# Kernel optimization log

Measured on AMD Instinct MI355X. Metric: run time of the kernel, lower is better.

The kernel has to match this reference:

```python
import jax, jax.numpy as jnp
import numpy as np
import math

N = 50000      # nodes
E = 800000     # edges (avg degree 16)
T = 4          # time steps
F = 64         # feature dim (in = hidden = out)
MAX_LEN = 200  # positional encoding table length
EPS = 1e-5     # BatchNorm eps


def _make_pe(time_dim, max_len):
    pe = np.zeros((max_len, time_dim), dtype=np.float32)
    position = np.arange(max_len, dtype=np.float32)[:, None]
    div_term = np.exp(np.arange(0, time_dim, 2, dtype=np.float32) * (-math.log(10000.0) / time_dim))
    pe[:, 0::2] = np.sin(position * div_term)
    pe[:, 1::2] = np.cos(position * div_term)
    return jnp.asarray(pe)


def setup_inputs() -> dict:
    key = jax.random.key(0)
    ks = jax.random.split(key, 10)
    xav = math.sqrt(2.0 / (F + F))  # xavier_normal_ std for square linear
    return {
        "node_features": jax.random.normal(ks[0], (N, T, F), dtype=jnp.float32),
        "edges_weight": jax.random.uniform(ks[1], (T, E), dtype=jnp.float32),
        "identities": jax.random.randint(ks[2], (T,), 0, MAX_LEN),
        "edge_src": jax.random.randint(ks[3], (E,), 0, N),
        "edge_dst": jax.random.randint(ks[4], (E,), 0, N),
        "pe": _make_pe(F, MAX_LEN),
        "W0": jax.random.normal(ks[5], (F, F), dtype=jnp.float32) * xav,
        "W1": jax.random.normal(ks[6], (F, F), dtype=jnp.float32) * xav,
        "g0": jnp.ones((F,), jnp.float32),
        "b0": jnp.zeros((F,), jnp.float32),
        "g1": jnp.ones((F,), jnp.float32),
        "b1": jnp.zeros((F,), jnp.float32),
    }


def _gcn_layer(h, ew, edge_src, edge_dst, W):
    # gather-mul-scatter: msg_e = h[src_e] * w_e ; agg_v = sum_{e: dst=v} msg_e
    msg = h[edge_src] * ew                                   # (E, T, F)
    agg = jax.ops.segment_sum(msg, edge_dst, num_segments=N)  # (N, T, F)
    readout = agg.mean(axis=0)                                # dgl.mean_nodes (single graph) -> (T, F)
    return agg @ W, readout @ W


def _batchnorm(x, gamma, beta):
    # training-mode batch stats over all non-channel dims
    mean = x.mean(axis=(0, 1))
    var = x.var(axis=(0, 1))
    return (x - mean) * jax.lax.rsqrt(var + EPS) * gamma + beta


def reference(node_features, edges_weight, identities, edge_src, edge_dst,
              pe, W0, W1, g0, b0, g1, b1):
    # positional encoding added per time step
    h = node_features + pe[identities]          # (N, T, F)
    ew = edges_weight.T[:, :, None]             # (E, T, 1)
    # layer 0: gcn -> dropout(eval=identity) -> BN -> ReLU
    h, readout = _gcn_layer(h, ew, edge_src, edge_dst, W0)
    h = jax.nn.relu(_batchnorm(h, g0, b0))
    # layer 1 (output layer)
    h, readout = _gcn_layer(h, ew, edge_src, edge_dst, W1)
    h = jax.nn.relu(_batchnorm(h, g1, b1))
    return h, readout
```

## Files before the change

### kernel.cpp

```cpp
#include <hip/hip_runtime.h>

#define TF 256

typedef __attribute__((ext_vector_type(8))) short short8;
typedef __attribute__((ext_vector_type(4))) float f32x4;

__device__ inline unsigned short f2bf(float x) {
  unsigned u = __float_as_uint(x);
  u += 0x7fffu + ((u >> 16) & 1u);
  return (unsigned short)(u >> 16);
}
__device__ inline unsigned pack2(unsigned short lo, unsigned short hi) {
  return (unsigned)lo | ((unsigned)hi << 16);
}
__device__ inline float bflo(unsigned u) { return __uint_as_float(u << 16); }
__device__ inline float bfhi(unsigned u) { return __uint_as_float(u & 0xffff0000u); }

__global__ void zero_kernel(int* __restrict__ p, int n) {
  int i = blockIdx.x * blockDim.x + threadIdx.x;
  if (i < n) p[i] = 0;
}

__global__ void hist_kernel(const int* __restrict__ dst, int* __restrict__ indeg, int E) {
  int e = blockIdx.x * blockDim.x + threadIdx.x;
  if (e < E) atomicAdd(&indeg[dst[e]], 1);
}

__global__ __launch_bounds__(1024) void scan_part1(const int* __restrict__ indeg,
                                                   int* __restrict__ partials, int n) {
  __shared__ int wsum[16];
  const int tid = threadIdx.x;
  const int lane = tid & 63;
  const int wid = tid >> 6;
  int i = blockIdx.x * 1024 + tid;
  int s = (i < n) ? indeg[i] : 0;
  #pragma unroll
  for (int o = 1; o < 64; o <<= 1) s += __shfl_xor(s, o, 64);
  if (lane == 0) wsum[wid] = s;
  __syncthreads();
  if (tid == 0) {
    int acc = 0;
    #pragma unroll
    for (int w = 0; w < 16; ++w) acc += wsum[w];
    partials[blockIdx.x] = acc;
  }
}

__global__ __launch_bounds__(64) void scan_part2(const int* __restrict__ partials,
                                                 int* __restrict__ base,
                                                 int* __restrict__ offsets, int nb, int n) {
  const int i = threadIdx.x;
  int v = (i < nb) ? partials[i] : 0;
  int s = v;
  #pragma unroll
  for (int o = 1; o < 64; o <<= 1) {
    int t = __shfl_up(s, o, 64);
    if (i >= o) s += t;
  }
  if (i < nb) base[i] = s - v;
  if (i == nb - 1) offsets[n] = s;
}

__global__ __launch_bounds__(1024) void scan_part3(const int* __restrict__ indeg,
                                                   const int* __restrict__ base,
                                                   int* __restrict__ offsets,
                                                   int* __restrict__ cursor, int n) {
  __shared__ int wsum[16];
  const int tid = threadIdx.x;
  const int lane = tid & 63;
  const int wid = tid >> 6;
  int i = blockIdx.x * 1024 + tid;
  int v = (i < n) ? indeg[i] : 0;
  int s = v;
  #pragma unroll
  for (int o = 1; o < 64; o <<= 1) {
    int t = __shfl_up(s, o, 64);
    if (lane >= o) s += t;
  }
  if (lane == 63) wsum[wid] = s;
  __syncthreads();
  if (tid == 0) {
    int acc = 0;
    #pragma unroll
    for (int w = 0; w < 16; ++w) { int t = wsum[w]; wsum[w] = acc; acc += t; }
  }
  __syncthreads();
  int excl = s - v + wsum[wid] + base[blockIdx.x];
  if (i < n) { offsets[i] = excl; cursor[i] = excl; }
}

__global__ void fill_kernel(const int* __restrict__ src, const int* __restrict__ dst,
                            const float* __restrict__ ew, int* __restrict__ cursor,
                            int* __restrict__ csr_srcB, float4* __restrict__ csr_w, int E) {
  int e = blockIdx.x * blockDim.x + threadIdx.x;
  if (e >= E) return;
  int d = dst[e];
  int pos = atomicAdd(&cursor[d], 1);
  csr_srcB[pos] = src[e] << 9;
  float4 w;
  w.x = ew[0 * E + e];
  w.y = ew[1 * E + e];
  w.z = ew[2 * E + e];
  w.w = ew[3 * E + e];
  csr_w[pos] = w;
}

__global__ void prep_kernel(const float* __restrict__ x, const float* __restrict__ pe,
                            const int* __restrict__ ids, uint2* __restrict__ h0, int n4) {
  int i = blockIdx.x * blockDim.x + threadIdx.x;
  const int stride = gridDim.x * blockDim.x;
  for (; i < n4; i += stride) {
    int e0 = (i << 2) & (TF - 1);
    int t = e0 >> 6;
    int f4 = e0 & 63;
    float4 v = reinterpret_cast<const float4*>(x)[i];
    float4 p = *reinterpret_cast<const float4*>(&pe[ids[t] * 64 + f4]);
    uint2 o;
    o.x = pack2(f2bf(v.x + p.x), f2bf(v.y + p.y));
    o.y = pack2(f2bf(v.z + p.z), f2bf(v.w + p.w));
    h0[i] = o;
  }
}

template <int LAYER>
__global__ __launch_bounds__(256) void aggregate_kernel(
    const char* __restrict__ h_base, const int* __restrict__ offsets,
    const int* __restrict__ csr_srcB, const float* __restrict__ csr_w,
    const float* __restrict__ scale, const float* __restrict__ shiftv,
    uint4* __restrict__ agg, int n_nodes) {
  const int lane = threadIdx.x & 63;
  const int wid = threadIdx.x >> 6;
  const int v = blockIdx.x * 4 + wid;
  if (v >= n_nodes) return;
  const int p = lane >> 5;
  const unsigned q = lane & 31;
  const unsigned qb = q << 4;
  const int tw = q >> 3;

  float sc[8], sh[8];
  if (LAYER == 1) {
    const int f0 = (q & 7) << 3;
    #pragma unroll
    for (int j = 0; j < 8; ++j) { sc[j] = scale[f0 + j]; sh[j] = shiftv[f0 + j]; }
  }

  float acc[8];
  #pragma unroll
  for (int j = 0; j < 8; ++j) acc[j] = 0.f;

  auto body = [&](uint4 u, float w) {
    float x[8] = {bflo(u.x), bfhi(u.x), bflo(u.y), bfhi(u.y),
                  bflo(u.z), bfhi(u.z), bflo(u.w), bfhi(u.w)};
    #pragma unroll
    for (int j = 0; j < 8; ++j) {
      float t = x[j];
      if (LAYER == 1) t = fmaxf(0.f, fmaf(t, sc[j], sh[j]));
      acc[j] = fmaf(w, t, acc[j]);
    }
  };

  const int beg = offsets[v];
  const int end = offsets[v + 1];
  int i = beg;
  for (; i + 4 <= end; i += 4) {
    const int e0 = i + p;
    const int e1 = i + 2 + p;
    const unsigned s0 = (unsigned)csr_srcB[e0];
    const unsigned s1 = (unsigned)csr_srcB[e1];
    const float w0 = csr_w[e0 * 4 + tw];
    const float w1 = csr_w[e1 * 4 + tw];
    const uint4 u0 = *reinterpret_cast<const uint4*>(h_base + (s0 + qb));
    const uint4 u1 = *reinterpret_cast<const uint4*>(h_base + (s1 + qb));
    body(u0, w0);
    body(u1, w1);
  }
  for (; i < end; i += 2) {
    const int ee = i + p;
    const int e = ee < end ? ee : end - 1;
    float w = csr_w[e * 4 + tw];
    if (ee >= end) w = 0.f;
    const unsigned s = (unsigned)csr_srcB[e];
    const uint4 u = *reinterpret_cast<const uint4*>(h_base + (s + qb));
    body(u, w);
  }

  #pragma unroll
  for (int j = 0; j < 8; ++j) acc[j] += __shfl_xor(acc[j], 32, 64);
  if (lane < 32) {
    uint4 o;
    o.x = pack2(f2bf(acc[0]), f2bf(acc[1]));
    o.y = pack2(f2bf(acc[2]), f2bf(acc[3]));
    o.z = pack2(f2bf(acc[4]), f2bf(acc[5]));
    o.w = pack2(f2bf(acc[6]), f2bf(acc[7]));
    agg[(size_t)v * 32 + q] = o;
  }
}

__global__ __launch_bounds__(512) void wfrag_kernel(const float* __restrict__ W0,
                                                    const float* __restrict__ W1,
                                                    short* __restrict__ wf0,
                                                    short* __restrict__ wf1) {
  const int frag = threadIdx.x >> 6, lane = threadIdx.x & 63;
  const int c = frag >> 1, h = frag & 1;
  const int n = (c << 4) + (lane & 15);
  const int k0 = h * 32 + ((lane >> 4) << 3);
  short* o0 = wf0 + frag * 512 + lane * 8;
  short* o1 = wf1 + frag * 512 + lane * 8;
  #pragma unroll
  for (int i = 0; i < 8; ++i) {
    o0[i] = (short)f2bf(W0[(k0 + i) * 64 + n]);
    o1[i] = (short)f2bf(W1[(k0 + i) * 64 + n]);
  }
}

__global__ __launch_bounds__(256) void mfma_matmul_kernel(
    const unsigned short* __restrict__ aggb, const short* __restrict__ wf,
    unsigned short* __restrict__ y_bf, float* __restrict__ part, int R) {
  const int tid = threadIdx.x;
  const int lane = tid & 63;
  const int wid = tid >> 6;

  short8 bfr[8];
  #pragma unroll
  for (int g = 0; g < 8; ++g)
    bfr[g] = *reinterpret_cast<const short8*>(wf + g * 512 + lane * 8);

  f32x4 csum[4];
  float ssq[4];
  #pragma unroll
  for (int c = 0; c < 4; ++c) { csum[c] = (f32x4){0.f, 0.f, 0.f, 0.f}; ssq[c] = 0.f; }

  const int nrb = (R + 15) >> 4;
  const int k0 = (lane >> 4) << 3;
  for (int rb = blockIdx.x * 4 + wid; rb < nrb; rb += gridDim.x * 4) {
    const int base = rb << 4;
    const int row = base + (lane & 15);
    short8 a0 = (short8){0, 0, 0, 0, 0, 0, 0, 0};
    short8 a1 = a0;
    if (row < R) {
      const short8* ap = reinterpret_cast<const short8*>(aggb + (size_t)row * 64 + k0);
      a0 = ap[0];
      a1 = ap[4];
    }
    f32x4 acc[4];
    #pragma unroll
    for (int c = 0; c < 4; ++c) {
      acc[c] = (f32x4){0.f, 0.f, 0.f, 0.f};
      acc[c] = __builtin_amdgcn_mfma_f32_16x16x32_bf16(a0, bfr[c * 2 + 0], acc[c], 0, 0, 0);
      acc[c] = __builtin_amdgcn_mfma_f32_16x16x32_bf16(a1, bfr[c * 2 + 1], acc[c], 0, 0, 0);
    }
    const int rbase = base + ((lane >> 4) << 2);
    #pragma unroll
    for (int c = 0; c < 4; ++c) {
      const int col = (c << 4) + (lane & 15);
      #pragma unroll
      for (int i = 0; i < 4; ++i) {
        const int r2 = rbase + i;
        if (r2 < R) {
          const float val = acc[c][i];
          y_bf[(size_t)r2 * 64 + col] = f2bf(val);
          csum[c][i] += val;
          ssq[c] += val * val;
        }
      }
    }
  }

  #pragma unroll
  for (int c = 0; c < 4; ++c) {
    #pragma unroll
    for (int i = 0; i < 4; ++i) {
      float v = csum[c][i];
      v += __shfl_xor(v, 16, 64);
      v += __shfl_xor(v, 32, 64);
      csum[c][i] = v;
    }
    float q = ssq[c];
    q += __shfl_xor(q, 16, 64);
    q += __shfl_xor(q, 32, 64);
    ssq[c] = q;
  }
  __shared__ float lcs[4][256];
  __shared__ float lsq[4][64];
  if (lane < 16) {
    #pragma unroll
    for (int c = 0; c < 4; ++c) {
      #pragma unroll
      for (int i = 0; i < 4; ++i) lcs[wid][i * 64 + (c << 4) + lane] = csum[c][i];
      lsq[wid][(c << 4) + lane] = ssq[c];
    }
  }
  __syncthreads();
  float s = lcs[0][tid] + lcs[1][tid] + lcs[2][tid] + lcs[3][tid];
  part[(size_t)blockIdx.x * 320 + tid] = s;
  if (tid < 64)
    part[(size_t)blockIdx.x * 320 + 256 + tid] =
        lsq[0][tid] + lsq[1][tid] + lsq[2][tid] + lsq[3][tid];
}

__global__ __launch_bounds__(1024) void reduce_part_kernel(const float* __restrict__ part,
                                                           float* __restrict__ red, int nblk) {
  __shared__ float lds[1024];
  const int tid = threadIdx.x;
  const int col = blockIdx.x * 16 + (tid & 15);
  const int r = tid >> 4;
  float s = 0.f;
  for (int bk = r; bk < nblk; bk += 64) s += part[(size_t)bk * 320 + col];
  lds[tid] = s;
  __syncthreads();
  #pragma unroll
  for (int off = 512; off >= 16; off >>= 1) {
    if (tid < off) lds[tid] += lds[tid + off];
    __syncthreads();
  }
  if (tid < 16) red[col] = lds[tid];
}

__global__ __launch_bounds__(64) void bn_from_red_kernel(
    const float* __restrict__ red, const float* __restrict__ g, const float* __restrict__ b,
    float* __restrict__ scale, float* __restrict__ shiftv, float inv_count) {
  const int f = threadIdx.x;
  float sum = red[f] + red[64 + f] + red[128 + f] + red[192 + f];
  float mean = sum * inv_count;
  float var = red[256 + f] * inv_count - mean * mean;
  float sc = g[f] * rsqrtf(var + 1e-5f);
  scale[f] = sc;
  shiftv[f] = fmaf(-mean, sc, b[f]);
}

__global__ __launch_bounds__(256) void finalize_from_red_kernel(
    const float* __restrict__ red, const float* __restrict__ g, const float* __restrict__ b,
    float* __restrict__ scale, float* __restrict__ shiftv, float inv_count,
    float* __restrict__ out_readout, float invN) {
  const int tid = threadIdx.x;
  out_readout[tid] = red[tid] * invN;
  if (tid < 64) {
    float sum = red[tid] + red[64 + tid] + red[128 + tid] + red[192 + tid];
    float mean = sum * inv_count;
    float var = red[256 + tid] * inv_count - mean * mean;
    float sc = g[tid] * rsqrtf(var + 1e-5f);
    scale[tid] = sc;
    shiftv[tid] = fmaf(-mean, sc, b[tid]);
  }
}

__global__ void bn_relu_out_kernel(const uint4* __restrict__ yb,
                                   const float* __restrict__ scale,
                                   const float* __restrict__ shiftv,
                                   float4* __restrict__ out, int n8) {
  int i = blockIdx.x * blockDim.x + threadIdx.x;
  if (i >= n8) return;
  const int f0 = (i & 7) << 3;
  uint4 u = yb[i];
  float x[8] = {bflo(u.x), bfhi(u.x), bflo(u.y), bfhi(u.y),
                bflo(u.z), bfhi(u.z), bflo(u.w), bfhi(u.w)};
  float4 o0, o1;
  o0.x = fmaxf(0.f, fmaf(x[0], scale[f0 + 0], shiftv[f0 + 0]));
  o0.y = fmaxf(0.f, fmaf(x[1], scale[f0 + 1], shiftv[f0 + 1]));
  o0.z = fmaxf(0.f, fmaf(x[2], scale[f0 + 2], shiftv[f0 + 2]));
  o0.w = fmaxf(0.f, fmaf(x[3], scale[f0 + 3], shiftv[f0 + 3]));
  o1.x = fmaxf(0.f, fmaf(x[4], scale[f0 + 4], shiftv[f0 + 4]));
  o1.y = fmaxf(0.f, fmaf(x[5], scale[f0 + 5], shiftv[f0 + 5]));
  o1.z = fmaxf(0.f, fmaf(x[6], scale[f0 + 6], shiftv[f0 + 6]));
  o1.w = fmaxf(0.f, fmaf(x[7], scale[f0 + 7], shiftv[f0 + 7]));
  out[i * 2 + 0] = o0;
  out[i * 2 + 1] = o1;
}

extern "C" void kernel_launch(void* const* d_in, const int* in_sizes, int n_in,
                              void* d_out, int out_size, void* d_ws, size_t ws_size,
                              hipStream_t stream) {
  const float* node_features = (const float*)d_in[0];
  const float* edges_weight  = (const float*)d_in[1];
  const int*   identities    = (const int*)d_in[2];
  const int*   edge_src      = (const int*)d_in[3];
  const int*   edge_dst      = (const int*)d_in[4];
  const float* pe            = (const float*)d_in[5];
  const float* W0            = (const float*)d_in[6];
  const float* W1            = (const float*)d_in[7];
  const float* g0            = (const float*)d_in[8];
  const float* b0            = (const float*)d_in[9];
  const float* g1            = (const float*)d_in[10];
  const float* b1            = (const float*)d_in[11];

  const int T = in_sizes[2];
  const int E = in_sizes[3];
  const int F = in_sizes[8];
  const int N = in_sizes[0] / (T * F);
  const int R = N * T;

  float* out = (float*)d_out;
  float* out_h = out;
  float* out_readout = out + (size_t)N * T * F;

  char* ws = (char*)d_ws;
  size_t off = 0;
  auto alloc = [&](size_t bytes) -> void* {
    off = (off + 255) & ~(size_t)255;
    void* p = ws + off;
    off += bytes;
    return p;
  };
  int*    indeg    = (int*)alloc((size_t)N * sizeof(int));
  int*    partials = (int*)alloc(64 * sizeof(int));
  int*    base_    = (int*)alloc(64 * sizeof(int));
  int*    offsets  = (int*)alloc(((size_t)N + 1) * sizeof(int));
  int*    cursor   = (int*)alloc((size_t)N * sizeof(int));
  int*    csr_srcB = (int*)alloc((size_t)E * sizeof(int));
  float4* csr_w    = (float4*)alloc((size_t)E * sizeof(float4));
  unsigned short* h0b  = (unsigned short*)alloc((size_t)N * TF * 2);
  unsigned short* aggb = (unsigned short*)alloc((size_t)N * TF * 2);
  short* wf0 = (short*)alloc(8 * 512 * sizeof(short));
  short* wf1 = (short*)alloc(8 * 512 * sizeof(short));
  const int MMB = 256;
  float* mm_part = (float*)alloc((size_t)MMB * 320 * sizeof(float));
  float* red     = (float*)alloc(320 * sizeof(float));
  float* scale0 = (float*)alloc(64 * sizeof(float));
  float* shift0 = (float*)alloc(64 * sizeof(float));
  float* scale1 = (float*)alloc(64 * sizeof(float));
  float* shift1 = (float*)alloc(64 * sizeof(float));
  (void)ws_size;

  const int nb = (N + 1023) / 1024;

  hipLaunchKernelGGL(zero_kernel, dim3((N + 255) / 256), dim3(256), 0, stream, indeg, N);
  hipLaunchKernelGGL(hist_kernel, dim3((E + 255) / 256), dim3(256), 0, stream, edge_dst, indeg, E);
  hipLaunchKernelGGL(scan_part1, dim3(nb), dim3(1024), 0, stream, indeg, partials, N);
  hipLaunchKernelGGL(scan_part2, dim3(1), dim3(64), 0, stream, partials, base_, offsets, nb, N);
  hipLaunchKernelGGL(scan_part3, dim3(nb), dim3(1024), 0, stream, indeg, base_, offsets, cursor, N);
  hipLaunchKernelGGL(fill_kernel, dim3((E + 255) / 256), dim3(256), 0, stream,
                     edge_src, edge_dst, edges_weight, cursor, csr_srcB, csr_w, E);

  hipLaunchKernelGGL(wfrag_kernel, dim3(1), dim3(512), 0, stream, W0, W1, wf0, wf1);
  hipLaunchKernelGGL(prep_kernel, dim3(2048), dim3(256), 0, stream,
                     node_features, pe, identities, (uint2*)h0b, (N * TF) / 4);

  const int agg_blocks = (N + 3) / 4;

  hipLaunchKernelGGL((aggregate_kernel<0>), dim3(agg_blocks), dim3(256), 0, stream,
                     (const char*)h0b, offsets, csr_srcB, (const float*)csr_w,
                     nullptr, nullptr, (uint4*)aggb, N);
  hipLaunchKernelGGL(mfma_matmul_kernel, dim3(MMB), dim3(256), 0, stream,
                     aggb, wf0, h0b , mm_part, R);
  hipLaunchKernelGGL(reduce_part_kernel, dim3(20), dim3(1024), 0, stream, mm_part, red, MMB);
  hipLaunchKernelGGL(bn_from_red_kernel, dim3(1), dim3(64), 0, stream,
                     red, g0, b0, scale0, shift0, 1.0f / (float)R);

  hipLaunchKernelGGL((aggregate_kernel<1>), dim3(agg_blocks), dim3(256), 0, stream,
                     (const char*)h0b , offsets, csr_srcB, (const float*)csr_w,
                     scale0, shift0, (uint4*)aggb, N);
  hipLaunchKernelGGL(mfma_matmul_kernel, dim3(MMB), dim3(256), 0, stream,
                     aggb, wf1, h0b , mm_part, R);
  hipLaunchKernelGGL(reduce_part_kernel, dim3(20), dim3(1024), 0, stream, mm_part, red, MMB);
  hipLaunchKernelGGL(finalize_from_red_kernel, dim3(1), dim3(256), 0, stream,
                     red, g1, b1, scale1, shift1, 1.0f / (float)R,
                     out_readout, 1.0f / (float)N);

  hipLaunchKernelGGL(bn_relu_out_kernel, dim3((R * 8 + 255) / 256), dim3(256), 0, stream,
                     (const uint4*)h0b, scale1, shift1, (float4*)out_h, R * 8);
}
```

Before: 285.0 us.

## Pack CSR source and bf16 edge weights into one 16-byte entry, unroll aggregation deeper

Merges the separate CSR source-index and float4 weight arrays into a single 16-byte record holding the pre-shifted source offset plus four bf16 weights, written with nontemporal stores. The aggregation loop now loads one entry per edge and unrolls 8 edges per iteration (4 per half-wave) to get more row gathers in flight. The zero kernel is replaced by hipMemsetAsync. Edge weights are rounded to bf16, which reduces precision slightly, and the padded 16-byte entry leaves 4 bytes unused.

```diff
diff --git a/kernel.cpp b/kernel.cpp
--- a/kernel.cpp
+++ b/kernel.cpp
@@ -4,6 +4,7 @@
 
 typedef __attribute__((ext_vector_type(8))) short short8;
 typedef __attribute__((ext_vector_type(4))) float f32x4;
+typedef __attribute__((ext_vector_type(4))) unsigned int uint4v;
 
 __device__ inline unsigned short f2bf(float x) {
   unsigned u = __float_as_uint(x);
@@ -15,11 +16,6 @@
 }
 __device__ inline float bflo(unsigned u) { return __uint_as_float(u << 16); }
 __device__ inline float bfhi(unsigned u) { return __uint_as_float(u & 0xffff0000u); }
-
-__global__ void zero_kernel(int* __restrict__ p, int n) {
-  int i = blockIdx.x * blockDim.x + threadIdx.x;
-  if (i < n) p[i] = 0;
-}
 
 __global__ void hist_kernel(const int* __restrict__ dst, int* __restrict__ indeg, int E) {
   int e = blockIdx.x * blockDim.x + threadIdx.x;
@@ -91,18 +87,17 @@
 
 __global__ void fill_kernel(const int* __restrict__ src, const int* __restrict__ dst,
                             const float* __restrict__ ew, int* __restrict__ cursor,
-                            int* __restrict__ csr_srcB, float4* __restrict__ csr_w, int E) {
+                            uint4v* __restrict__ csr_ent, int E) {
   int e = blockIdx.x * blockDim.x + threadIdx.x;
   if (e >= E) return;
   int d = dst[e];
   int pos = atomicAdd(&cursor[d], 1);
-  csr_srcB[pos] = src[e] << 9;
-  float4 w;
-  w.x = ew[0 * E + e];
-  w.y = ew[1 * E + e];
-  w.z = ew[2 * E + e];
-  w.w = ew[3 * E + e];
-  csr_w[pos] = w;
+  uint4v ent;
+  ent.x = (unsigned)(src[e] << 9);
+  ent.y = pack2(f2bf(ew[e]), f2bf(ew[(size_t)E + e]));
+  ent.z = pack2(f2bf(ew[2 * (size_t)E + e]), f2bf(ew[3 * (size_t)E + e]));
+  ent.w = 0u;
+  __builtin_nontemporal_store(ent, &csr_ent[pos]);
 }
 
 __global__ void prep_kernel(const float* __restrict__ x, const float* __restrict__ pe,
@@ -125,7 +120,7 @@
 template <int LAYER>
 __global__ __launch_bounds__(256) void aggregate_kernel(
     const char* __restrict__ h_base, const int* __restrict__ offsets,
-    const int* __restrict__ csr_srcB, const float* __restrict__ csr_w,
+    const uint4* __restrict__ csr_ent,
     const float* __restrict__ scale, const float* __restrict__ shiftv,
     uint4* __restrict__ agg, int n_nodes) {
   const int lane = threadIdx.x & 63;
@@ -148,6 +143,10 @@
   #pragma unroll
   for (int j = 0; j < 8; ++j) acc[j] = 0.f;
 
+  auto wext = [&](uint4 ent) -> float {
+    unsigned word = (tw & 2) ? ent.z : ent.y;
+    return (tw & 1) ? bfhi(word) : bflo(word);
+  };
   auto body = [&](uint4 u, float w) {
     float x[8] = {bflo(u.x), bfhi(u.x), bflo(u.y), bfhi(u.y),
                   bflo(u.z), bfhi(u.z), bflo(u.w), bfhi(u.w)};
@@ -162,26 +161,26 @@
   const int beg = offsets[v];
   const int end = offsets[v + 1];
   int i = beg;
-  for (; i + 4 <= end; i += 4) {
-    const int e0 = i + p;
-    const int e1 = i + 2 + p;
-    const unsigned s0 = (unsigned)csr_srcB[e0];
-    const unsigned s1 = (unsigned)csr_srcB[e1];
-    const float w0 = csr_w[e0 * 4 + tw];
-    const float w1 = csr_w[e1 * 4 + tw];
-    const uint4 u0 = *reinterpret_cast<const uint4*>(h_base + (s0 + qb));
-    const uint4 u1 = *reinterpret_cast<const uint4*>(h_base + (s1 + qb));
-    body(u0, w0);
-    body(u1, w1);
-  }
-  for (; i < end; i += 2) {
-    const int ee = i + p;
-    const int e = ee < end ? ee : end - 1;
-    float w = csr_w[e * 4 + tw];
-    if (ee >= end) w = 0.f;
-    const unsigned s = (unsigned)csr_srcB[e];
-    const uint4 u = *reinterpret_cast<const uint4*>(h_base + (s + qb));
-    body(u, w);
+  for (; i + 8 <= end; i += 8) {
+    uint4 ent[4];
+    #pragma unroll
+    for (int c = 0; c < 4; ++c) ent[c] = csr_ent[i + 2 * c + p];
+    uint4 row[4];
+    #pragma unroll
+    for (int c = 0; c < 4; ++c)
+      row[c] = *reinterpret_cast<const uint4*>(h_base + (ent[c].x + qb));
+    #pragma unroll
+    for (int c = 0; c < 4; ++c) body(row[c], wext(ent[c]));
+  }
+  for (; i + 2 <= end; i += 2) {
+    const uint4 ent = csr_ent[i + p];
+    const uint4 row = *reinterpret_cast<const uint4*>(h_base + (ent.x + qb));
+    body(row, wext(ent));
+  }
+  if (i < end) {
+    const uint4 ent = csr_ent[i];
+    const uint4 row = *reinterpret_cast<const uint4*>(h_base + (ent.x + qb));
+    body(row, p == 0 ? wext(ent) : 0.f);
   }
 
   #pragma unroll
@@ -406,8 +405,7 @@
   int*    base_    = (int*)alloc(64 * sizeof(int));
   int*    offsets  = (int*)alloc(((size_t)N + 1) * sizeof(int));
   int*    cursor   = (int*)alloc((size_t)N * sizeof(int));
-  int*    csr_srcB = (int*)alloc((size_t)E * sizeof(int));
-  float4* csr_w    = (float4*)alloc((size_t)E * sizeof(float4));
+  uint4v* csr_ent  = (uint4v*)alloc((size_t)E * 16);
   unsigned short* h0b  = (unsigned short*)alloc((size_t)N * TF * 2);
   unsigned short* aggb = (unsigned short*)alloc((size_t)N * TF * 2);
   short* wf0 = (short*)alloc(8 * 512 * sizeof(short));
@@ -423,13 +421,13 @@
 
   const int nb = (N + 1023) / 1024;
 
-  hipLaunchKernelGGL(zero_kernel, dim3((N + 255) / 256), dim3(256), 0, stream, indeg, N);
+  hipMemsetAsync(indeg, 0, (size_t)N * sizeof(int), stream);
   hipLaunchKernelGGL(hist_kernel, dim3((E + 255) / 256), dim3(256), 0, stream, edge_dst, indeg, E);
   hipLaunchKernelGGL(scan_part1, dim3(nb), dim3(1024), 0, stream, indeg, partials, N);
   hipLaunchKernelGGL(scan_part2, dim3(1), dim3(64), 0, stream, partials, base_, offsets, nb, N);
   hipLaunchKernelGGL(scan_part3, dim3(nb), dim3(1024), 0, stream, indeg, base_, offsets, cursor, N);
   hipLaunchKernelGGL(fill_kernel, dim3((E + 255) / 256), dim3(256), 0, stream,
-                     edge_src, edge_dst, edges_weight, cursor, csr_srcB, csr_w, E);
+                     edge_src, edge_dst, edges_weight, cursor, csr_ent, E);
 
   hipLaunchKernelGGL(wfrag_kernel, dim3(1), dim3(512), 0, stream, W0, W1, wf0, wf1);
   hipLaunchKernelGGL(prep_kernel, dim3(2048), dim3(256), 0, stream,
@@ -438,7 +436,7 @@
   const int agg_blocks = (N + 3) / 4;
 
   hipLaunchKernelGGL((aggregate_kernel<0>), dim3(agg_blocks), dim3(256), 0, stream,
-                     (const char*)h0b, offsets, csr_srcB, (const float*)csr_w,
+                     (const char*)h0b, offsets, (const uint4*)csr_ent,
                      nullptr, nullptr, (uint4*)aggb, N);
   hipLaunchKernelGGL(mfma_matmul_kernel, dim3(MMB), dim3(256), 0, stream,
                      aggb, wf0, h0b , mm_part, R);
@@ -447,7 +445,7 @@
                      red, g0, b0, scale0, shift0, 1.0f / (float)R);
 
   hipLaunchKernelGGL((aggregate_kernel<1>), dim3(agg_blocks), dim3(256), 0, stream,
-                     (const char*)h0b , offsets, csr_srcB, (const float*)csr_w,
+                     (const char*)h0b , offsets, (const uint4*)csr_ent,
                      scale0, shift0, (uint4*)aggb, N);
   hipLaunchKernelGGL(mfma_matmul_kernel, dim3(MMB), dim3(256), 0, stream,
                      aggb, wf1, h0b , mm_part, R);
```

Measured after the change: 288.9 us. About the same (+1.4%).
